# Performance work log

Hardware: AMD Instinct MI355X
Metric: run time of the kernel (lower is better)

The kernel has to match this reference:

```python
import jax, jax.numpy as jnp
import numpy as np

N = 131072      # evaluation batch
D = 512         # feature dim
NUM_BINS = 64


def setup_inputs() -> dict:
    key = jax.random.key(0)
    k_in, k_fr = jax.random.split(key)
    inputs = jax.random.normal(k_in, (N, D), dtype=jnp.float32)
    # positive frequencies so hist_probs > 0 and log() is finite
    frequencies = jax.random.uniform(k_fr, (NUM_BINS, D), dtype=jnp.float32) + 0.01
    # per-feature monotonically increasing bin edges covering the randn range
    base = jnp.linspace(-4.0, 4.0, NUM_BINS + 1, dtype=jnp.float32)
    edges = jnp.tile(base[:, None], (1, D))  # [num_bins+1, D]
    return {"inputs": inputs, "frequencies": frequencies, "edges": edges}


def reference(inputs, frequencies, edges):
    num_bins = frequencies.shape[0]
    # hist_probs[b, d] = P(bin b | feature d)
    hist_probs = frequencies / jnp.sum(frequencies, axis=0, keepdims=True)
    # tfp.stats.find_bins with extend_lower/upper_interval:
    # per-feature searchsorted, clipped into [0, num_bins-1]
    find = jax.vmap(lambda e, x: jnp.searchsorted(e, x, side="right"),
                    in_axes=(1, 1), out_axes=1)
    bin_idx = jnp.clip(find(edges, inputs) - 1, 0, num_bins - 1)  # [N, D] int
    # gather_nd: probabilities[n, d] = hist_probs[bin_idx[n, d], d]
    probabilities = jnp.take_along_axis(hist_probs, bin_idx, axis=0)  # [N, D]
    logits = jnp.sum(jnp.log(probabilities), axis=1)  # [N]
    logits = logits - jnp.mean(logits)
    return jax.nn.softmax(logits)  # softmax over the batch axis, shape [N]
```

## Files before the change

### kernel.cpp

```cpp
#include <hip/hip_runtime.h>
#include <math.h>

#define NROWS_DEF 131072
#define D 512
#define NB 64

#define OFF_LHG   0
#define OFF_SPAR  (NB*D)
#define OFF_CPAR  (OFF_SPAR + D)
#define OFF_BMAX  (OFF_CPAR + D)
#define OFF_GSUM  (OFF_BMAX + 256)

__device__ __forceinline__ int imin(int a, int b) { return a < b ? a : b; }
__device__ __forceinline__ int imax(int a, int b) { return a > b ? a : b; }

__global__ __launch_bounds__(256) void k_prep(const float* __restrict__ freq,
                                              const float* __restrict__ edges,
                                              float* __restrict__ ws) {
    int d = blockIdx.x * 256 + threadIdx.x;
    if (d >= D) return;
    float sum = 0.f;
    for (int b = 0; b < NB; ++b) sum += freq[b * D + d];
    for (int b = 0; b < NB; ++b)
        ws[OFF_LHG + b * D + d] = logf(freq[b * D + d] / sum);

    float e0 = edges[d], e64 = edges[NB * D + d];
    float s = (float)NB / (e64 - e0);
    float c = -e0 * s;
    bool ok = (e64 > e0) && isfinite(s) && isfinite(c);
    float prev = e0;
    for (int b = 1; b <= NB; ++b) { float e = edges[b * D + d]; ok = ok && (e > prev); prev = e; }
    for (int b = 0; b <= NB; ++b) {
        float t = fmaf(edges[b * D + d], s, c);
        ok = ok && (fabsf(t - (float)b) < 2e-5f);
    }
    ws[OFF_SPAR + d] = ok ? s : __int_as_float(0x7fc00000);
    ws[OFF_CPAR + d] = c;
}

__device__ __forceinline__ int careful_bin(const float* __restrict__ edges, int d, float x) {
    int lo = 0, hi = NB + 1;
    while (lo < hi) {
        int mid = (lo + hi) >> 1;
        float e = edges[mid * D + d];
        if (e <= x) lo = mid + 1; else hi = mid;
    }
    return imin(NB - 1, imax(0, lo - 1));
}

__device__ __forceinline__ int bin_of(float x, float s, float c,
                                      const float* __restrict__ edges, int d) {
    float t  = fmaf(x, s, c);
    float fl = floorf(t);
    float fr = t - fl;
    int b = imin(NB - 1, imax(0, (int)fl));
    if (!((fr >= 1e-4f) && (fr <= 0.9999f)))
        b = careful_bin(edges, d, x);
    return b;
}

__global__ __launch_bounds__(1024, 4) void k_main(const float* __restrict__ in,
                                                  const float* __restrict__ edges,
                                                  const float* __restrict__ ws,
                                                  float* __restrict__ logits,
                                                  int nrows) {
    extern __shared__ float lh[];
    for (int idx = threadIdx.x; idx < NB * D; idx += 1024) {
        int b = idx >> 9;
        int d = idx & (D - 1);
        lh[d * 65 + b] = ws[OFF_LHG + idx];
    }
    __syncthreads();

    const int lane = threadIdx.x & 63;
    const int wid  = threadIdx.x >> 6;

    float s[8], c[8];
    int   lb[8], dd[8];
    #pragma unroll
    for (int j = 0; j < 8; ++j) {
        int d = lane + 64 * j;
        dd[j] = d;
        s[j]  = ws[OFF_SPAR + d];
        c[j]  = ws[OFF_CPAR + d];
        lb[j] = d * 65;
    }

    const int r0 = blockIdx.x * 512;
    for (int r = r0 + wid * 2; r < r0 + 512; r += 32) {
        bool do0 = (r < nrows), do1 = (r + 1 < nrows);
        const float* rp0 = in + (size_t)r * D + lane;
        const float* rp1 = rp0 + D;
        float x0[8], x1[8];
        #pragma unroll
        for (int j = 0; j < 8; ++j) x0[j] = do0 ? rp0[64 * j] : 0.f;
        #pragma unroll
        for (int j = 0; j < 8; ++j) x1[j] = do1 ? rp1[64 * j] : 0.f;

        float a0 = 0.f, a1 = 0.f;
        #pragma unroll
        for (int j = 0; j < 8; ++j) {
            a0 += lh[lb[j] + bin_of(x0[j], s[j], c[j], edges, dd[j])];
            a1 += lh[lb[j] + bin_of(x1[j], s[j], c[j], edges, dd[j])];
        }
        #pragma unroll
        for (int off = 32; off > 0; off >>= 1) {
            a0 += __shfl_down(a0, off);
            a1 += __shfl_down(a1, off);
        }
        if (lane == 0) {
            if (do0) logits[r]     = a0;
            if (do1) logits[r + 1] = a1;
        }
    }
}

__global__ __launch_bounds__(256) void k_max(const float* __restrict__ logits,
                                             float* __restrict__ bmax, int n) {
    int tid = blockIdx.x * 256 + threadIdx.x;
    float m = -INFINITY;
    for (int i = tid; i < n; i += 256 * 256) m = fmaxf(m, logits[i]);
    #pragma unroll
    for (int off = 32; off > 0; off >>= 1) m = fmaxf(m, __shfl_down(m, off));
    __shared__ float sm[4];
    int lane = threadIdx.x & 63, wid = threadIdx.x >> 6;
    if (lane == 0) sm[wid] = m;
    __syncthreads();
    if (threadIdx.x == 0)
        bmax[blockIdx.x] = fmaxf(fmaxf(sm[0], sm[1]), fmaxf(sm[2], sm[3]));
}

__global__ __launch_bounds__(256) void k_exp(float* __restrict__ io,
                                             const float* __restrict__ bmax,
                                             float* __restrict__ gsum, int n) {
    __shared__ float sm[4];
    int lane = threadIdx.x & 63, wid = threadIdx.x >> 6;
    float m = bmax[threadIdx.x];
    #pragma unroll
    for (int off = 32; off > 0; off >>= 1) m = fmaxf(m, __shfl_down(m, off));
    if (lane == 0) sm[wid] = m;
    __syncthreads();
    float gmax = fmaxf(fmaxf(sm[0], sm[1]), fmaxf(sm[2], sm[3]));
    __syncthreads();

    int tid = blockIdx.x * 256 + threadIdx.x;
    float lsum = 0.f;
    for (int i = tid; i < n; i += 256 * 256) {
        float e = expf(io[i] - gmax);
        io[i] = e;
        lsum += e;
    }
    #pragma unroll
    for (int off = 32; off > 0; off >>= 1) lsum += __shfl_down(lsum, off);
    if (lane == 0) sm[wid] = lsum;
    __syncthreads();
    if (threadIdx.x == 0) atomicAdd(gsum, sm[0] + sm[1] + sm[2] + sm[3]);
}

__global__ __launch_bounds__(256) void k_scale(float* __restrict__ io,
                                               const float* __restrict__ gsum, int n) {
    float r = 1.0f / *gsum;
    int tid = blockIdx.x * 256 + threadIdx.x;
    for (int i = tid; i < n; i += 256 * 256) io[i] *= r;
}

extern "C" void kernel_launch(void* const* d_in, const int* in_sizes, int n_in,
                              void* d_out, int out_size, void* d_ws, size_t ws_size,
                              hipStream_t stream) {
    const float* inputs = (const float*)d_in[0];
    const float* freq   = (const float*)d_in[1];
    const float* edges  = (const float*)d_in[2];
    float* out = (float*)d_out;
    float* ws  = (float*)d_ws;
    const int nrows = in_sizes[0] / D;

    hipMemsetAsync((char*)d_ws + OFF_GSUM * sizeof(float), 0, sizeof(float), stream);

    k_prep<<<(D + 255) / 256, 256, 0, stream>>>(freq, edges, ws);

    const int lds_bytes = D * 65 * sizeof(float);
    hipFuncSetAttribute((const void*)k_main,
                        hipFuncAttributeMaxDynamicSharedMemorySize, lds_bytes);
    int nblk = (nrows + 511) / 512;
    k_main<<<nblk, 1024, lds_bytes, stream>>>(inputs, edges, ws, out, nrows);

    k_max<<<256, 256, 0, stream>>>(out, ws + OFF_BMAX, nrows);
    k_exp<<<256, 256, 0, stream>>>(out, ws + OFF_BMAX, ws + OFF_GSUM, nrows);
    k_scale<<<256, 256, 0, stream>>>(out, ws + OFF_GSUM, nrows);
}
```

Measured before the change: 402.8 us.

## Fuse online softmax max/sum into main kernel and simplify bin fallback

The main kernel now keeps a per-wave online max and rescaled exp-sum, writes them as partials, and a single-block combine merges them. This replaces the separate max, exp and scale passes with one combine plus one vectorized exp-and-normalize pass. The main loop handles 4 rows per wave per iteration to raise memory-level parallelism. Near-edge inputs now fall back to a one-edge check instead of a full binary search. The extra per-row expf in the main kernel and the modified edge tolerance are the trade-offs.

```diff
diff --git a/kernel.cpp b/kernel.cpp
--- a/kernel.cpp
+++ b/kernel.cpp
@@ -1,28 +1,28 @@
 #include <hip/hip_runtime.h>
 #include <math.h>
 
-#define NROWS_DEF 131072
 #define D 512
 #define NB 64
 
 #define OFF_LHG   0
 #define OFF_SPAR  (NB*D)
 #define OFF_CPAR  (OFF_SPAR + D)
-#define OFF_BMAX  (OFF_CPAR + D)
-#define OFF_GSUM  (OFF_BMAX + 256)
-
-__device__ __forceinline__ int imin(int a, int b) { return a < b ? a : b; }
-__device__ __forceinline__ int imax(int a, int b) { return a > b ? a : b; }
-
-__global__ __launch_bounds__(256) void k_prep(const float* __restrict__ freq,
+#define OFF_PART  (OFF_CPAR + D)
+#define MAXPART   16384
+#define OFF_RES   (OFF_PART + 2*MAXPART)
+
+static __device__ __forceinline__ int imin(int a, int b) { return a < b ? a : b; }
+static __device__ __forceinline__ int imax(int a, int b) { return a > b ? a : b; }
+
+__global__ __launch_bounds__(512) void k_prep(const float* __restrict__ freq,
                                               const float* __restrict__ edges,
                                               float* __restrict__ ws) {
-    int d = blockIdx.x * 256 + threadIdx.x;
-    if (d >= D) return;
+    int d = threadIdx.x;
     float sum = 0.f;
     for (int b = 0; b < NB; ++b) sum += freq[b * D + d];
+    float inv = 1.0f / sum;
     for (int b = 0; b < NB; ++b)
-        ws[OFF_LHG + b * D + d] = logf(freq[b * D + d] / sum);
+        ws[OFF_LHG + b * D + d] = logf(freq[b * D + d] * inv);
 
     float e0 = edges[d], e64 = edges[NB * D + d];
     float s = (float)NB / (e64 - e0);
@@ -38,7 +38,8 @@
     ws[OFF_CPAR + d] = c;
 }
 
-__device__ __forceinline__ int careful_bin(const float* __restrict__ edges, int d, float x) {
+static __device__ __forceinline__ int careful_bin(const float* __restrict__ edges,
+                                                  int d, float x) {
     int lo = 0, hi = NB + 1;
     while (lo < hi) {
         int mid = (lo + hi) >> 1;
@@ -48,22 +49,30 @@
     return imin(NB - 1, imax(0, lo - 1));
 }
 
-__device__ __forceinline__ int bin_of(float x, float s, float c,
-                                      const float* __restrict__ edges, int d) {
+static __device__ __forceinline__ int bin_of(float x, float s, float c,
+                                             const float* __restrict__ edges, int d) {
     float t  = fmaf(x, s, c);
     float fl = floorf(t);
     float fr = t - fl;
     int b = imin(NB - 1, imax(0, (int)fl));
-    if (!((fr >= 1e-4f) && (fr <= 0.9999f)))
-        b = careful_bin(edges, d, x);
+    if (__builtin_expect(!(fr >= 4e-5f && fr <= 0.99996f), 0)) {
+        if (!__builtin_isnan(s)) {
+            int kk = imin(NB, imax(0, (int)rintf(t)));
+            float e = edges[kk * D + d];
+            b = imin(NB - 1, imax(0, (x >= e) ? kk : kk - 1));
+        } else {
+            b = careful_bin(edges, d, x);
+        }
+    }
     return b;
 }
 
-__global__ __launch_bounds__(1024, 4) void k_main(const float* __restrict__ in,
-                                                  const float* __restrict__ edges,
-                                                  const float* __restrict__ ws,
-                                                  float* __restrict__ logits,
-                                                  int nrows) {
+__global__ __launch_bounds__(1024) void k_main(const float* __restrict__ in,
+                                               const float* __restrict__ edges,
+                                               const float* __restrict__ ws,
+                                               float* __restrict__ logits,
+                                               float* __restrict__ part,
+                                               int nrows) {
     extern __shared__ float lh[];
     for (int idx = threadIdx.x; idx < NB * D; idx += 1024) {
         int b = idx >> 9;
@@ -75,93 +84,126 @@
     const int lane = threadIdx.x & 63;
     const int wid  = threadIdx.x >> 6;
 
-    float s[8], c[8];
-    int   lb[8], dd[8];
+    float s[8], c[8]; int lb[8];
     #pragma unroll
     for (int j = 0; j < 8; ++j) {
         int d = lane + 64 * j;
-        dd[j] = d;
         s[j]  = ws[OFF_SPAR + d];
         c[j]  = ws[OFF_CPAR + d];
         lb[j] = d * 65;
     }
 
+    float m = -INFINITY, ssum = 0.f;
     const int r0 = blockIdx.x * 512;
-    for (int r = r0 + wid * 2; r < r0 + 512; r += 32) {
-        bool do0 = (r < nrows), do1 = (r + 1 < nrows);
-        const float* rp0 = in + (size_t)r * D + lane;
-        const float* rp1 = rp0 + D;
-        float x0[8], x1[8];
+    const bool full = (r0 + 512 <= nrows);
+
+    for (int k = 0; k < 8; ++k) {
+        const int r = r0 + wid * 4 + k * 64;
+        if (full || r + 4 <= nrows) {
+            const float* rp = in + (size_t)r * D + lane;
+            float x[4][8];
+            #pragma unroll
+            for (int i = 0; i < 4; ++i)
+                #pragma unroll
+                for (int j = 0; j < 8; ++j)
+                    x[i][j] = rp[i * D + 64 * j];
+            float a[4] = {0.f, 0.f, 0.f, 0.f};
+            #pragma unroll
+            for (int i = 0; i < 4; ++i)
+                #pragma unroll
+                for (int j = 0; j < 8; ++j)
+                    a[i] += lh[lb[j] + bin_of(x[i][j], s[j], c[j], edges, lane + 64 * j)];
+            #pragma unroll
+            for (int i = 0; i < 4; ++i)
+                #pragma unroll
+                for (int off = 32; off; off >>= 1)
+                    a[i] += __shfl_xor(a[i], off);
+            if (lane == 0) {
+                logits[r]     = a[0];
+                logits[r + 1] = a[1];
+                logits[r + 2] = a[2];
+                logits[r + 3] = a[3];
+            }
+            #pragma unroll
+            for (int i = 0; i < 4; ++i) {
+                float mo = m;
+                m = fmaxf(m, a[i]);
+                ssum = ssum * __expf(mo - m) + __expf(a[i] - m);
+            }
+        } else {
+            for (int i = 0; i < 4; ++i) {
+                int rr = r + i;
+                if (rr >= nrows) break;
+                const float* rp = in + (size_t)rr * D + lane;
+                float a = 0.f;
+                #pragma unroll
+                for (int j = 0; j < 8; ++j)
+                    a += lh[lb[j] + bin_of(rp[64 * j], s[j], c[j], edges, lane + 64 * j)];
+                #pragma unroll
+                for (int off = 32; off; off >>= 1) a += __shfl_xor(a, off);
+                if (lane == 0) logits[rr] = a;
+                float mo = m;
+                m = fmaxf(m, a);
+                ssum = ssum * __expf(mo - m) + __expf(a - m);
+            }
+        }
+    }
+    if (lane == 0) {
+        int w = blockIdx.x * 16 + wid;
+        part[2 * w]     = m;
+        part[2 * w + 1] = ssum;
+    }
+}
+
+__global__ __launch_bounds__(1024) void k_combine(const float* __restrict__ part,
+                                                  float* __restrict__ res, int npart) {
+    float m = -INFINITY, s = 0.f;
+    for (int i = threadIdx.x; i < npart; i += 1024) {
+        float pm = part[2 * i], ps = part[2 * i + 1];
+        float mn = fmaxf(m, pm);
+        if (mn > -INFINITY) s = s * __expf(m - mn) + ps * __expf(pm - mn);
+        m = mn;
+    }
+    #pragma unroll
+    for (int off = 32; off; off >>= 1) {
+        float pm = __shfl_xor(m, off), ps = __shfl_xor(s, off);
+        float mn = fmaxf(m, pm);
+        if (mn > -INFINITY) s = s * __expf(m - mn) + ps * __expf(pm - mn);
+        else s = 0.f;
+        m = mn;
+    }
+    __shared__ float sm[16][2];
+    int lane = threadIdx.x & 63, wid = threadIdx.x >> 6;
+    if (lane == 0) { sm[wid][0] = m; sm[wid][1] = s; }
+    __syncthreads();
+    if (wid == 0) {
+        m = (lane < 16) ? sm[lane][0] : -INFINITY;
+        s = (lane < 16) ? sm[lane][1] : 0.f;
         #pragma unroll
-        for (int j = 0; j < 8; ++j) x0[j] = do0 ? rp0[64 * j] : 0.f;
-        #pragma unroll
-        for (int j = 0; j < 8; ++j) x1[j] = do1 ? rp1[64 * j] : 0.f;
-
-        float a0 = 0.f, a1 = 0.f;
-        #pragma unroll
-        for (int j = 0; j < 8; ++j) {
-            a0 += lh[lb[j] + bin_of(x0[j], s[j], c[j], edges, dd[j])];
-            a1 += lh[lb[j] + bin_of(x1[j], s[j], c[j], edges, dd[j])];
+        for (int off = 8; off; off >>= 1) {
+            float pm = __shfl_xor(m, off), ps = __shfl_xor(s, off);
+            float mn = fmaxf(m, pm);
+            if (mn > -INFINITY) s = s * __expf(m - mn) + ps * __expf(pm - mn);
+            else s = 0.f;
+            m = mn;
         }
-        #pragma unroll
-        for (int off = 32; off > 0; off >>= 1) {
-            a0 += __shfl_down(a0, off);
-            a1 += __shfl_down(a1, off);
-        }
-        if (lane == 0) {
-            if (do0) logits[r]     = a0;
-            if (do1) logits[r + 1] = a1;
-        }
-    }
-}
-
-__global__ __launch_bounds__(256) void k_max(const float* __restrict__ logits,
-                                             float* __restrict__ bmax, int n) {
-    int tid = blockIdx.x * 256 + threadIdx.x;
-    float m = -INFINITY;
-    for (int i = tid; i < n; i += 256 * 256) m = fmaxf(m, logits[i]);
-    #pragma unroll
-    for (int off = 32; off > 0; off >>= 1) m = fmaxf(m, __shfl_down(m, off));
-    __shared__ float sm[4];
-    int lane = threadIdx.x & 63, wid = threadIdx.x >> 6;
-    if (lane == 0) sm[wid] = m;
-    __syncthreads();
-    if (threadIdx.x == 0)
-        bmax[blockIdx.x] = fmaxf(fmaxf(sm[0], sm[1]), fmaxf(sm[2], sm[3]));
-}
-
-__global__ __launch_bounds__(256) void k_exp(float* __restrict__ io,
-                                             const float* __restrict__ bmax,
-                                             float* __restrict__ gsum, int n) {
-    __shared__ float sm[4];
-    int lane = threadIdx.x & 63, wid = threadIdx.x >> 6;
-    float m = bmax[threadIdx.x];
-    #pragma unroll
-    for (int off = 32; off > 0; off >>= 1) m = fmaxf(m, __shfl_down(m, off));
-    if (lane == 0) sm[wid] = m;
-    __syncthreads();
-    float gmax = fmaxf(fmaxf(sm[0], sm[1]), fmaxf(sm[2], sm[3]));
-    __syncthreads();
-
-    int tid = blockIdx.x * 256 + threadIdx.x;
-    float lsum = 0.f;
-    for (int i = tid; i < n; i += 256 * 256) {
-        float e = expf(io[i] - gmax);
-        io[i] = e;
-        lsum += e;
-    }
-    #pragma unroll
-    for (int off = 32; off > 0; off >>= 1) lsum += __shfl_down(lsum, off);
-    if (lane == 0) sm[wid] = lsum;
-    __syncthreads();
-    if (threadIdx.x == 0) atomicAdd(gsum, sm[0] + sm[1] + sm[2] + sm[3]);
-}
-
-__global__ __launch_bounds__(256) void k_scale(float* __restrict__ io,
-                                               const float* __restrict__ gsum, int n) {
-    float r = 1.0f / *gsum;
-    int tid = blockIdx.x * 256 + threadIdx.x;
-    for (int i = tid; i < n; i += 256 * 256) io[i] *= r;
+        if (lane == 0) { res[0] = m; res[1] = 1.0f / s; }
+    }
+}
+
+__global__ __launch_bounds__(256) void k_final(float* __restrict__ io,
+                                               const float* __restrict__ res, int n) {
+    float M = res[0], invS = res[1];
+    float2* io2 = (float2*)io;
+    int n2 = n >> 1;
+    for (int idx = blockIdx.x * 256 + threadIdx.x; idx < n2; idx += gridDim.x * 256) {
+        float2 v = io2[idx];
+        v.x = __expf(v.x - M) * invS;
+        v.y = __expf(v.y - M) * invS;
+        io2[idx] = v;
+    }
+    if (blockIdx.x == 0 && threadIdx.x == 0 && (n & 1))
+        io[n - 1] = __expf(io[n - 1] - M) * invS;
 }
 
 extern "C" void kernel_launch(void* const* d_in, const int* in_sizes, int n_in,
@@ -173,18 +215,17 @@
     float* out = (float*)d_out;
     float* ws  = (float*)d_ws;
     const int nrows = in_sizes[0] / D;
-
-    hipMemsetAsync((char*)d_ws + OFF_GSUM * sizeof(float), 0, sizeof(float), stream);
-
-    k_prep<<<(D + 255) / 256, 256, 0, stream>>>(freq, edges, ws);
+    const int nblk  = (nrows + 511) / 512;
+    const int npart = nblk * 16;
+
+    k_prep<<<1, 512, 0, stream>>>(freq, edges, ws);
 
     const int lds_bytes = D * 65 * sizeof(float);
     hipFuncSetAttribute((const void*)k_main,
                         hipFuncAttributeMaxDynamicSharedMemorySize, lds_bytes);
-    int nblk = (nrows + 511) / 512;
-    k_main<<<nblk, 1024, lds_bytes, stream>>>(inputs, edges, ws, out, nrows);
-
-    k_max<<<256, 256, 0, stream>>>(out, ws + OFF_BMAX, nrows);
-    k_exp<<<256, 256, 0, stream>>>(out, ws + OFF_BMAX, ws + OFF_GSUM, nrows);
-    k_scale<<<256, 256, 0, stream>>>(out, ws + OFF_GSUM, nrows);
-}
+    k_main<<<nblk, 1024, lds_bytes, stream>>>(inputs, edges, ws, out,
+                                              ws + OFF_PART, nrows);
+
+    k_combine<<<1, 1024, 0, stream>>>(ws + OFF_PART, ws + OFF_RES, npart);
+    k_final<<<256, 256, 0, stream>>>(out, ws + OFF_RES, nrows);
+}
```

Result: faster. 388.1 us (-3.7%).
